# Kernel tuning notes

Hardware: AMD Instinct MI355X
Metric: run time of the kernel (lower is better)

Reference implementation:

```python
import jax, jax.numpy as jnp
import numpy as np

H, KVH, D, HID = 32, 8, 128, 4096
ROPE_LEN, THETA = 8192, 10000.0
MASK_OUT, MIN_REMAIN = 0.9, 128


def _rope_tables(dtype):
    inv_freq = 1.0 / (THETA ** (jnp.arange(0, D, 2, dtype=jnp.float32) / D))
    freqs = jnp.arange(ROPE_LEN, dtype=jnp.float32)[:, None] * inv_freq[None, :]
    emb = jnp.concatenate([freqs, freqs], axis=-1)  # [8192, 128]
    return jnp.cos(emb).astype(dtype), jnp.sin(emb).astype(dtype)


def _rotate_half(x):
    x1, x2 = x[..., : D // 2], x[..., D // 2:]
    return jnp.concatenate([-x2, x1], axis=-1)


def _apply_rope(x, pos, cos, sin):
    c, s = cos[pos][None, None], sin[pos][None, None]  # [1,1,L,D]
    return x * c + _rotate_half(x) * s


def setup_inputs() -> dict:
    key = jax.random.key(0)
    ks = jax.random.split(key, 11)
    S = 4096
    f = jnp.float32
    return {
        "hidden_states": jax.random.normal(ks[0], (1, 1, HID), f),
        "key_cache": jax.random.normal(ks[1], (1, H, S, D), f),
        "val_cache": jax.random.normal(ks[2], (1, H, S, D), f),
        "Wq": jax.random.normal(ks[3], (HID, HID), f) * 0.02,
        "Wk": jax.random.normal(ks[4], (HID, KVH * D), f) * 0.02,
        "Wv": jax.random.normal(ks[5], (HID, KVH * D), f) * 0.02,
        "Wo": jax.random.normal(ks[6], (HID, HID), f) * 0.02,
        "hash_proj1": jax.random.normal(ks[7], (1, H, D, D), f) * 0.001,
        "hash_bias1": jnp.zeros((1, H, 1, D), f),
        "hash_proj2": jax.random.normal(ks[8], (1, H, D, D), f) * 0.001,
        "hash_bias2": jnp.zeros((1, H, 1, D), f),
    }


def reference(hidden_states, key_cache, val_cache, Wq, Wk, Wv, Wo,
              hash_proj1, hash_bias1, hash_proj2, hash_bias2):
    B, Q, _ = hidden_states.shape  # B=1, Q=1 (decode step)
    G = H // KVH
    dtype = hidden_states.dtype

    # projections -> [B, heads, Q, D]
    ques = (hidden_states @ Wq).reshape(B, Q, H, D).transpose(0, 2, 1, 3)
    k_new = (hidden_states @ Wk).reshape(B, Q, KVH, D).transpose(0, 2, 1, 3)
    v_new = (hidden_states @ Wv).reshape(B, Q, KVH, D).transpose(0, 2, 1, 3)
    k_new = jnp.repeat(k_new, G, axis=1)  # repeat_kv
    v_new = jnp.repeat(v_new, G, axis=1)

    keys = jnp.concatenate([key_cache, k_new], axis=2)  # [1,H,K,D]
    vals = jnp.concatenate([val_cache, v_new], axis=2)
    K = keys.shape[2]

    cos, sin = _rope_tables(dtype)
    q_pos = K - Q + jnp.arange(Q)
    k_pos = jnp.arange(K)
    q_r = _apply_rope(ques, q_pos, cos, sin)
    k_r = _apply_rope(keys, k_pos, cos, sin)

    # per-head hash MLP: silu layer with residue, then linear layer with residue
    def hash_fn(x):
        h = jax.nn.silu(jnp.einsum('bhld,bhde->bhle', x, hash_proj1) + hash_bias1) + x
        h = (jnp.einsum('bhld,bhde->bhle', h, hash_proj2) + hash_bias2) + h
        return h

    q_hash = jnp.sign(hash_fn(q_r))
    k_hash = jnp.sign(hash_fn(k_r))
    draft_score = jnp.einsum('bhqd,bhkd->bhqk', q_hash, k_hash)  # LSH similarity

    num_remain = max(min(K, MIN_REMAIN), K - int(K * MASK_OUT))
    _, idx = jax.lax.top_k(draft_score, num_remain)  # [B,H,Q,num_remain]

    neg = jnp.finfo(dtype).min
    mask = jnp.full((B, H, Q, K), neg, dtype=dtype)
    bi = jnp.arange(B)[:, None, None, None]
    hi = jnp.arange(H)[None, :, None, None]
    qi = jnp.arange(Q)[None, None, :, None]
    mask = mask.at[bi, hi, qi, idx].set(0.0)

    scores = jnp.einsum('bhqd,bhkd->bhqk', q_r, k_r) / np.sqrt(D) + mask
    attn = jax.nn.softmax(scores, axis=-1)
    out = jnp.einsum('bhqk,bhkd->bhqd', attn, vals)
    out = out.transpose(0, 2, 1, 3).reshape(B, Q, HID) @ Wo
    return out
```

## Files before the change

### kernel.cpp

```cpp
#include <hip/hip_runtime.h>
#include <math.h>

#define NH 32
#define NKVH 8
#define HD 128

typedef _Float16 half8 __attribute__((ext_vector_type(8)));
typedef float f32x4 __attribute__((ext_vector_type(4)));

#define OFF_QPROJ 0
#define OFF_KNEW  4096
#define OFF_VNEW  5120
#define OFF_QR    6144
#define OFF_QHASH 10240
#define OFF_TAB   10368

__global__ void init_kernel(const float* __restrict__ hp1, const float* __restrict__ hp2,
                            float* __restrict__ ws, float* __restrict__ out,
                            int K, int nInit) {
    const int tid = threadIdx.x;
    if ((int)blockIdx.x < nInit) {
        int idx = blockIdx.x * 256 + tid;
        if (idx < K * 64) {
            int pos = idx >> 6, d = idx & 63;
            double inv = exp(-((double)d / 64.0) * log(10000.0));
            double ang = (double)pos * inv;
            double s, c;
            sincos(ang, &s, &c);
            ws[OFF_TAB + idx]                  = (float)c;
            ws[OFF_TAB + (size_t)K * 64 + idx] = (float)s;
        }
        if (idx < 6144) ws[OFF_QPROJ + idx] = 0.f;
        if (idx < 4096) out[idx] = 0.f;
        size_t off_attn = OFF_TAB + 2 * (size_t)K * 64 + 2 * (size_t)NH * K;
        if (idx < 4096) ws[off_attn + idx] = 0.f;
    } else {
        int id = blockIdx.x - nInit;
        int h2 = id >> 3;
        int tg = (id & 7) * 256 + tid;
        const int lane = tg & 63, nt = (tg >> 6) & 7, ks = tg >> 9;
        const int kbase = ks * 32 + ((tg >> 4) & 3) * 8;
        const int n = nt * 16 + (tg & 15);
        const float* P = ((h2 & 1) ? hp2 : hp1) + (size_t)(h2 >> 1) * 16384;
        half8 v;
#pragma unroll
        for (int j = 0; j < 8; ++j) v[j] = (_Float16)P[(size_t)(kbase + j) * 128 + n];
        size_t off_pt = OFF_TAB + 2 * (size_t)K * 64 + 2 * (size_t)NH * K + 4096 + 2 * (size_t)NH * 512;
        ((half8*)(ws + off_pt))[(size_t)h2 * 2048 + tg] = v;
    }
}

__global__ __launch_bounds__(256) void qkv_gemv(const float* __restrict__ hidden,
        const float* __restrict__ Wq, const float* __restrict__ Wk,
        const float* __restrict__ Wv, float* __restrict__ ws) {
    __shared__ float hs[64];
    const int tid = threadIdx.x;
    const int col = (blockIdx.x * 256 + tid) * 4;
    const int i0  = blockIdx.y * 64;
    if (tid < 64) hs[tid] = hidden[i0 + tid];
    __syncthreads();
    const float* W; int ld, wcol;
    if (col < 4096)      { W = Wq; ld = 4096; wcol = col; }
    else if (col < 5120) { W = Wk; ld = 1024; wcol = col - 4096; }
    else                 { W = Wv; ld = 1024; wcol = col - 5120; }
    const float* p = W + (size_t)i0 * ld + wcol;
    float4 a0 = {0.f,0.f,0.f,0.f}, a1 = {0.f,0.f,0.f,0.f};
#pragma unroll 4
    for (int ii = 0; ii < 64; ii += 2) {
        float4 w0 = *(const float4*)p;
        float4 w1 = *(const float4*)(p + ld);
        float h0 = hs[ii], h1 = hs[ii + 1];
        a0.x = fmaf(h0, w0.x, a0.x); a0.y = fmaf(h0, w0.y, a0.y);
        a0.z = fmaf(h0, w0.z, a0.z); a0.w = fmaf(h0, w0.w, a0.w);
        a1.x = fmaf(h1, w1.x, a1.x); a1.y = fmaf(h1, w1.y, a1.y);
        a1.z = fmaf(h1, w1.z, a1.z); a1.w = fmaf(h1, w1.w, a1.w);
        p += 2 * (size_t)ld;
    }
    atomicAdd(&ws[OFF_QPROJ + col + 0], a0.x + a1.x);
    atomicAdd(&ws[OFF_QPROJ + col + 1], a0.y + a1.y);
    atomicAdd(&ws[OFF_QPROJ + col + 2], a0.z + a1.z);
    atomicAdd(&ws[OFF_QPROJ + col + 3], a0.w + a1.w);
}

__global__ __launch_bounds__(128) void qhash_kernel(const float* __restrict__ hp1,
        const float* __restrict__ hb1, const float* __restrict__ hp2,
        const float* __restrict__ hb2, float* __restrict__ ws, int S) {
    const int h = blockIdx.x, d = threadIdx.x;
    const int K = S + 1;
    __shared__ float X[128], H1[128];
    float q  = ws[OFF_QPROJ + h * 128 + d];
    float qp = ws[OFF_QPROJ + h * 128 + (d ^ 64)];
    const float* cosT = ws + OFF_TAB;
    const float* sinT = cosT + (size_t)K * 64;
    float cs = cosT[(size_t)S * 64 + (d & 63)];
    float sn = sinT[(size_t)S * 64 + (d & 63)];
    float r = (d < 64) ? -qp : qp;
    float qr = q * cs + r * sn;
    X[d] = qr;
    ws[OFF_QR + h * 128 + d] = qr;
    __syncthreads();
    const float* P1 = hp1 + (size_t)h * 16384;
    float t = hb1[h * 128 + d];
    for (int i = 0; i < 128; ++i) t = fmaf(X[i], P1[i * 128 + d], t);
    float u = t / (1.f + expf(-t)) + X[d];
    H1[d] = u;
    __syncthreads();
    const float* P2 = hp2 + (size_t)h * 16384;
    float t2 = hb2[h * 128 + d] + u;
    for (int i = 0; i < 128; ++i) t2 = fmaf(H1[i], P2[i * 128 + d], t2);
    unsigned long long bal = __ballot(t2 > 0.f);
    if ((d & 63) == 0)
        ((unsigned long long*)(ws + OFF_QHASH))[h * 2 + (d >> 6)] = bal;
}

__global__ __launch_bounds__(256, 3) void key_kernel(const float* __restrict__ key_cache,
        const float* __restrict__ hb1, const float* __restrict__ hb2,
        float* __restrict__ ws, int S) {
    const int K  = S + 1;
    const int h  = blockIdx.y;
    const int k0 = blockIdx.x * 64;
    const int tid = threadIdx.x;
    const int wv = tid >> 6, lane = tid & 63;
    const int m = lane & 15, quad = lane >> 4;

    __shared__ float    XF[64 * 132];
    __shared__ _Float16 XH[64 * 136];

    const float* cosT = ws + OFF_TAB;
    const float* sinT = cosT + (size_t)K * 64;
    float* scores = ws + OFF_TAB + 2 * (size_t)K * 64;
    int*   draft  = (int*)(scores + (size_t)NH * K);
    size_t off_pt = OFF_TAB + 2 * (size_t)K * 64 + 2 * (size_t)NH * K + 4096 + 2 * (size_t)NH * 512;
    const half8* PT1 = (const half8*)((const _Float16*)(ws + off_pt) + (size_t)(h * 2) * 16384);
    const half8* PT2 = PT1 + 2048;

    const int key = tid >> 2, qq = tid & 3, d0 = qq * 16;
    const int kg = k0 + key;
    float lo[16], hi[16];
    if (kg < K) {
        const float* row = (kg < S) ? key_cache + ((size_t)h * S + kg) * 128
                                    : ws + OFF_KNEW + (h >> 2) * 128;
#pragma unroll
        for (int i4 = 0; i4 < 4; ++i4) {
            float4 xa = *(const float4*)(row + d0 + i4 * 4);
            float4 xb = *(const float4*)(row + 64 + d0 + i4 * 4);
            float4 cc = *(const float4*)(cosT + (size_t)kg * 64 + d0 + i4 * 4);
            float4 ss = *(const float4*)(sinT + (size_t)kg * 64 + d0 + i4 * 4);
            lo[i4*4+0] = xa.x * cc.x - xb.x * ss.x;  hi[i4*4+0] = xb.x * cc.x + xa.x * ss.x;
            lo[i4*4+1] = xa.y * cc.y - xb.y * ss.y;  hi[i4*4+1] = xb.y * cc.y + xa.y * ss.y;
            lo[i4*4+2] = xa.z * cc.z - xb.z * ss.z;  hi[i4*4+2] = xb.z * cc.z + xa.z * ss.z;
            lo[i4*4+3] = xa.w * cc.w - xb.w * ss.w;  hi[i4*4+3] = xb.w * cc.w + xa.w * ss.w;
        }
    } else {
#pragma unroll
        for (int i = 0; i < 16; ++i) { lo[i] = 0.f; hi[i] = 0.f; }
    }
#pragma unroll
    for (int i4 = 0; i4 < 4; ++i4) {
        float4 l4 = {lo[i4*4], lo[i4*4+1], lo[i4*4+2], lo[i4*4+3]};
        float4 h4 = {hi[i4*4], hi[i4*4+1], hi[i4*4+2], hi[i4*4+3]};
        *(float4*)&XF[key * 132 + d0 + i4 * 4]      = l4;
        *(float4*)&XF[key * 132 + 64 + d0 + i4 * 4] = h4;
    }
    {
        half8 hl0, hl1, hh0, hh1;
#pragma unroll
        for (int i = 0; i < 8; ++i) {
            hl0[i] = (_Float16)lo[i];     hl1[i] = (_Float16)lo[8 + i];
            hh0[i] = (_Float16)hi[i];     hh1[i] = (_Float16)hi[8 + i];
        }
        *(half8*)&XH[key * 136 + d0]          = hl0;
        *(half8*)&XH[key * 136 + d0 + 8]      = hl1;
        *(half8*)&XH[key * 136 + 64 + d0]     = hh0;
        *(half8*)&XH[key * 136 + 64 + d0 + 8] = hh1;
    }

    {
        const float* qr = ws + OFF_QR + h * 128;
        float part = 0.f;
#pragma unroll
        for (int i4 = 0; i4 < 4; ++i4) {
            float4 qa = *(const float4*)(qr + d0 + i4 * 4);
            float4 qb = *(const float4*)(qr + 64 + d0 + i4 * 4);
            part = fmaf(qa.x, lo[i4*4+0], fmaf(qb.x, hi[i4*4+0], part));
            part = fmaf(qa.y, lo[i4*4+1], fmaf(qb.y, hi[i4*4+1], part));
            part = fmaf(qa.z, lo[i4*4+2], fmaf(qb.z, hi[i4*4+2], part));
            part = fmaf(qa.w, lo[i4*4+3], fmaf(qb.w, hi[i4*4+3], part));
        }
        part += __shfl_xor(part, 1);
        part += __shfl_xor(part, 2);
        if (qq == 0 && kg < K) scores[(size_t)h * K + kg] = part * 0.08838834764831845f;
    }

    float b1v[8], b2v[8];
#pragma unroll
    for (int nt = 0; nt < 8; ++nt) {
        b1v[nt] = hb1[h * 128 + nt * 16 + m];
        b2v[nt] = hb2[h * 128 + nt * 16 + m];
    }
    unsigned short qh16[8];
    {
        uint4 q4 = *(const uint4*)((const unsigned*)(ws + OFF_QHASH) + h * 4);
        unsigned qa[4] = {q4.x, q4.y, q4.z, q4.w};
#pragma unroll
        for (int nt = 0; nt < 8; ++nt)
            qh16[nt] = (unsigned short)((qa[nt >> 1] >> ((nt & 1) * 16)) & 0xFFFFu);
    }

    f32x4 acc[8];

#define GEMM_MFMA(PT)                                                              \
    {                                                                              \
        _Pragma("unroll") for (int nt = 0; nt < 8; ++nt)                           \
            acc[nt] = (f32x4){0.f, 0.f, 0.f, 0.f};                                 \
        _Pragma("unroll") for (int c = 0; c < 4; ++c) {                            \
            half8 afrag = *(const half8*)&XH[(wv * 16 + m) * 136 + c * 32 + quad * 8]; \
            _Pragma("unroll") for (int nt = 0; nt < 8; ++nt) {                     \
                half8 bfrag = (PT)[c * 512 + nt * 64 + lane];                      \
                acc[nt] = __builtin_amdgcn_mfma_f32_16x16x32_f16(afrag, bfrag, acc[nt], 0, 0, 0); \
            }                                                                      \
        }                                                                          \
    }

    GEMM_MFMA(PT1)
#pragma unroll
    for (int nt = 0; nt < 8; ++nt) {
        const int n = nt * 16 + m;
#pragma unroll
        for (int r = 0; r < 4; ++r) {
            const int kk = wv * 16 + quad * 4 + r;
            float t = acc[nt][r] + b1v[nt];
            float x = XF[kk * 132 + n];
            float h1v = t / (1.f + expf(-t)) + x;
            XF[kk * 132 + n] = h1v;
            XH[kk * 136 + n] = (_Float16)h1v;
        }
    }

    GEMM_MFMA(PT2)
    {
        int ham[4] = {0, 0, 0, 0};
#pragma unroll
        for (int nt = 0; nt < 8; ++nt) {
            const int n = nt * 16 + m;
#pragma unroll
            for (int r = 0; r < 4; ++r) {
                const int kk = wv * 16 + quad * 4 + r;
                float t2 = acc[nt][r] + b2v[nt] + XF[kk * 132 + n];
                unsigned long long bal = __ballot(t2 > 0.f);
                unsigned bits = (unsigned)(bal >> (quad * 16)) & 0xFFFFu;
                ham[r] += __popc(bits ^ (unsigned)qh16[nt]);
            }
        }
        if (m == 0) {
#pragma unroll
            for (int r = 0; r < 4; ++r) {
                int kgd = k0 + wv * 16 + quad * 4 + r;
                if (kgd < K) draft[(size_t)h * K + kgd] = 128 - 2 * ham[r];
            }
        }
    }
#undef GEMM_MFMA
}

__global__ __launch_bounds__(256) void select_kernel(float* __restrict__ ws, int S, int nrem) {
    const int K = S + 1;
    const int h = blockIdx.x;
    const int tid = threadIdx.x;
    __shared__ int hist[129];
    __shared__ int sel_idx[512];
    __shared__ float red[256];
    __shared__ int wtot[4];
    __shared__ int sh_tval, sh_r, sh_cnt, sh_run;

    float* scoresB = ws + OFF_TAB + 2 * (size_t)K * 64;
    const int* draft = (const int*)(scoresB + (size_t)NH * K) + (size_t)h * K;
    const float* sc = scoresB + (size_t)h * K;
    float* attn = scoresB + 2 * (size_t)NH * K;
    int*   selidx_g = (int*)(attn + 4096) + h * 512;
    float* selw_g   = (attn + 4096 + NH * 512) + h * 512;

    for (int i = tid; i < 129; i += 256) hist[i] = 0;
    if (tid == 0) { sh_cnt = 0; sh_run = 0; }
    __syncthreads();
    for (int k = tid; k < K; k += 256) atomicAdd(&hist[(draft[k] + 128) >> 1], 1);
    __syncthreads();
    if (tid == 0) {
        int cum = 0, tb = 0, r = nrem;
        for (int b = 128; b >= 0; --b) {
            int c = hist[b];
            if (cum + c >= nrem) { tb = b; r = nrem - cum; break; }
            cum += c;
        }
        sh_tval = tb * 2 - 128; sh_r = r;
    }
    __syncthreads();
    const int tval = sh_tval, r = sh_r;
    const int lane = tid & 63, wave = tid >> 6;
    for (int base = 0; base < K; base += 256) {
        int k = base + tid;
        bool valid = (k < K);
        int dv = valid ? draft[k] : -1000;
        bool eq = valid && (dv == tval);
        bool gt = valid && (dv > tval);
        unsigned long long bal = __ballot(eq);
        if (lane == 0) wtot[wave] = __popcll(bal);
        __syncthreads();
        int woff = 0;
        for (int w = 0; w < wave; ++w) woff += wtot[w];
        int rank = sh_run + woff + __popcll(bal & ((1ull << lane) - 1ull));
        bool sel = gt || (eq && (rank < r));
        if (sel) sel_idx[atomicAdd(&sh_cnt, 1)] = k;
        __syncthreads();
        if (tid == 0) sh_run += wtot[0] + wtot[1] + wtot[2] + wtot[3];
        __syncthreads();
    }
    float mmax = -3.402823466e38f;
    for (int li = tid; li < nrem; li += 256) mmax = fmaxf(mmax, sc[sel_idx[li]]);
    red[tid] = mmax; __syncthreads();
    for (int s2 = 128; s2 > 0; s2 >>= 1) {
        if (tid < s2) red[tid] = fmaxf(red[tid], red[tid + s2]);
        __syncthreads();
    }
    mmax = red[0]; __syncthreads();
    float z = 0.f;
    for (int li = tid; li < nrem; li += 256) z += expf(sc[sel_idx[li]] - mmax);
    red[tid] = z; __syncthreads();
    for (int s2 = 128; s2 > 0; s2 >>= 1) {
        if (tid < s2) red[tid] += red[tid + s2];
        __syncthreads();
    }
    float Z = red[0]; __syncthreads();
    for (int li = tid; li < nrem; li += 256) {
        int idx = sel_idx[li];
        selidx_g[li] = idx;
        selw_g[li] = expf(sc[idx] - mmax) / Z;
    }
}

__global__ __launch_bounds__(256) void gather_kernel(const float* __restrict__ val_cache,
        float* __restrict__ ws, int S, int nrem) {
    const int K = S + 1;
    const int h = blockIdx.x, g = blockIdx.y;
    const int tid = threadIdx.x;
    const int wave = tid >> 6, lane = tid & 63;
    const int stream = g * 4 + wave;
    float* scoresB = ws + OFF_TAB + 2 * (size_t)K * 64;
    float* attn = scoresB + 2 * (size_t)NH * K;
    const int*   selidx_g = (const int*)(attn + 4096) + h * 512;
    const float* selw_g   = (attn + 4096 + NH * 512) + h * 512;
    float ax = 0.f, ay = 0.f;
    for (int li = stream; li < nrem; li += 64) {
        int idx = selidx_g[li];
        float w = selw_g[li];
        const float* vr = (idx < S) ? val_cache + ((size_t)h * S + idx) * 128
                                    : ws + OFF_VNEW + (h >> 2) * 128;
        float2 v = ((const float2*)vr)[lane];
        ax = fmaf(w, v.x, ax);
        ay = fmaf(w, v.y, ay);
    }
    atomicAdd(&attn[h * 128 + lane * 2 + 0], ax);
    atomicAdd(&attn[h * 128 + lane * 2 + 1], ay);
}

__global__ __launch_bounds__(256) void out_gemv(const float* __restrict__ Wo,
        const float* __restrict__ ws, float* __restrict__ out, int K) {
    __shared__ float hs[64];
    const int tid = threadIdx.x;
    const int col = (blockIdx.x * 256 + tid) * 4;
    const int i0  = blockIdx.y * 64;
    const float* ao = ws + OFF_TAB + 2 * (size_t)K * 64 + 2 * (size_t)NH * K;
    if (tid < 64) hs[tid] = ao[i0 + tid];
    __syncthreads();
    const float* p = Wo + (size_t)i0 * 4096 + col;
    float4 a0 = {0.f,0.f,0.f,0.f}, a1 = {0.f,0.f,0.f,0.f};
#pragma unroll 4
    for (int ii = 0; ii < 64; ii += 2) {
        float4 w0 = *(const float4*)p;
        float4 w1 = *(const float4*)(p + 4096);
        float h0 = hs[ii], h1 = hs[ii + 1];
        a0.x = fmaf(h0, w0.x, a0.x); a0.y = fmaf(h0, w0.y, a0.y);
        a0.z = fmaf(h0, w0.z, a0.z); a0.w = fmaf(h0, w0.w, a0.w);
        a1.x = fmaf(h1, w1.x, a1.x); a1.y = fmaf(h1, w1.y, a1.y);
        a1.z = fmaf(h1, w1.z, a1.z); a1.w = fmaf(h1, w1.w, a1.w);
        p += 8192;
    }
    atomicAdd(&out[col + 0], a0.x + a1.x);
    atomicAdd(&out[col + 1], a0.y + a1.y);
    atomicAdd(&out[col + 2], a0.z + a1.z);
    atomicAdd(&out[col + 3], a0.w + a1.w);
}

extern "C" void kernel_launch(void* const* d_in, const int* in_sizes, int n_in,
                              void* d_out, int out_size, void* d_ws, size_t ws_size,
                              hipStream_t stream) {
    const float* hidden = (const float*)d_in[0];
    const float* key_cache = (const float*)d_in[1];
    const float* val_cache = (const float*)d_in[2];
    const float* Wq = (const float*)d_in[3];
    const float* Wk = (const float*)d_in[4];
    const float* Wv = (const float*)d_in[5];
    const float* Wo = (const float*)d_in[6];
    const float* hp1 = (const float*)d_in[7];
    const float* hb1 = (const float*)d_in[8];
    const float* hp2 = (const float*)d_in[9];
    const float* hb2 = (const float*)d_in[10];
    float* out = (float*)d_out;
    float* ws  = (float*)d_ws;

    const int S = in_sizes[1] / (NH * HD);
    const int K = S + 1;
    int mn = (K < 128) ? K : 128;
    int nrem = K - (int)((double)K * 0.9);
    if (nrem < mn) nrem = mn;

    const int nInit = (K * 64 + 255) / 256;
    init_kernel<<<nInit + 512, 256, 0, stream>>>(hp1, hp2, ws, out, K, nInit);
    qkv_gemv<<<dim3(6, 64), 256, 0, stream>>>(hidden, Wq, Wk, Wv, ws);
    qhash_kernel<<<NH, 128, 0, stream>>>(hp1, hb1, hp2, hb2, ws, S);
    key_kernel<<<dim3((K + 63) / 64, NH), 256, 0, stream>>>(key_cache, hb1, hb2, ws, S);
    select_kernel<<<NH, 256, 0, stream>>>(ws, S, nrem);
    gather_kernel<<<dim3(NH, 16), 256, 0, stream>>>(val_cache, ws, S, nrem);
    out_gemv<<<dim3(4, 64), 256, 0, stream>>>(Wo, ws, out, K);
}
```

Baseline: 346.1 us.

## Process two key tiles per block with prefetch, direct MFMA fragments, swizzled LDS

key_kernel now handles 128 keys per block as two 64-key tiles, loading the second tile's key rows before the first tile is processed so global latency overlaps compute. Each lane loads its key data directly in MFMA A-fragment layout, which removes the fp16 shared staging buffer, and the fp32 LDS buffer uses an XOR swizzle instead of padding. Shared memory shrinks and occupancy bounds rise to 4, at the cost of more registers held for the prefetched tile and half as many blocks.

```diff
diff --git a/kernel.cpp b/kernel.cpp
--- a/kernel.cpp
+++ b/kernel.cpp
@@ -113,18 +113,20 @@
         ((unsigned long long*)(ws + OFF_QHASH))[h * 2 + (d >> 6)] = bal;
 }
 
-__global__ __launch_bounds__(256, 3) void key_kernel(const float* __restrict__ key_cache,
+__global__ __launch_bounds__(256, 4) void key_kernel(const float* __restrict__ key_cache,
         const float* __restrict__ hb1, const float* __restrict__ hb2,
         float* __restrict__ ws, int S) {
     const int K  = S + 1;
     const int h  = blockIdx.y;
-    const int k0 = blockIdx.x * 64;
+    const int k0 = blockIdx.x * 128;
     const int tid = threadIdx.x;
     const int wv = tid >> 6, lane = tid & 63;
     const int m = lane & 15, quad = lane >> 4;
-
-    __shared__ float    XF[64 * 132];
-    __shared__ _Float16 XH[64 * 136];
+    const int row = wv * 16 + m;
+    const int cbase = quad * 8;
+    const int sw = (m & 7) << 2;
+
+    __shared__ float XF[64 * 128];
 
     const float* cosT = ws + OFF_TAB;
     const float* sinT = cosT + (size_t)K * 64;
@@ -134,70 +136,119 @@
     const half8* PT1 = (const half8*)((const _Float16*)(ws + off_pt) + (size_t)(h * 2) * 16384);
     const half8* PT2 = PT1 + 2048;
 
-    const int key = tid >> 2, qq = tid & 3, d0 = qq * 16;
-    const int kg = k0 + key;
-    float lo[16], hi[16];
-    if (kg < K) {
-        const float* row = (kg < S) ? key_cache + ((size_t)h * S + kg) * 128
-                                    : ws + OFF_KNEW + (h >> 2) * 128;
-#pragma unroll
-        for (int i4 = 0; i4 < 4; ++i4) {
-            float4 xa = *(const float4*)(row + d0 + i4 * 4);
-            float4 xb = *(const float4*)(row + 64 + d0 + i4 * 4);
-            float4 cc = *(const float4*)(cosT + (size_t)kg * 64 + d0 + i4 * 4);
-            float4 ss = *(const float4*)(sinT + (size_t)kg * 64 + d0 + i4 * 4);
-            lo[i4*4+0] = xa.x * cc.x - xb.x * ss.x;  hi[i4*4+0] = xb.x * cc.x + xa.x * ss.x;
-            lo[i4*4+1] = xa.y * cc.y - xb.y * ss.y;  hi[i4*4+1] = xb.y * cc.y + xa.y * ss.y;
-            lo[i4*4+2] = xa.z * cc.z - xb.z * ss.z;  hi[i4*4+2] = xb.z * cc.z + xa.z * ss.z;
-            lo[i4*4+3] = xa.w * cc.w - xb.w * ss.w;  hi[i4*4+3] = xb.w * cc.w + xa.w * ss.w;
-        }
-    } else {
-#pragma unroll
-        for (int i = 0; i < 16; ++i) { lo[i] = 0.f; hi[i] = 0.f; }
-    }
-#pragma unroll
-    for (int i4 = 0; i4 < 4; ++i4) {
-        float4 l4 = {lo[i4*4], lo[i4*4+1], lo[i4*4+2], lo[i4*4+3]};
-        float4 h4 = {hi[i4*4], hi[i4*4+1], hi[i4*4+2], hi[i4*4+3]};
-        *(float4*)&XF[key * 132 + d0 + i4 * 4]      = l4;
-        *(float4*)&XF[key * 132 + 64 + d0 + i4 * 4] = h4;
-    }
-    {
-        half8 hl0, hl1, hh0, hh1;
-#pragma unroll
-        for (int i = 0; i < 8; ++i) {
-            hl0[i] = (_Float16)lo[i];     hl1[i] = (_Float16)lo[8 + i];
-            hh0[i] = (_Float16)hi[i];     hh1[i] = (_Float16)hi[8 + i];
-        }
-        *(half8*)&XH[key * 136 + d0]          = hl0;
-        *(half8*)&XH[key * 136 + d0 + 8]      = hl1;
-        *(half8*)&XH[key * 136 + 64 + d0]     = hh0;
-        *(half8*)&XH[key * 136 + 64 + d0 + 8] = hh1;
-    }
-
-    {
-        const float* qr = ws + OFF_QR + h * 128;
-        float part = 0.f;
-#pragma unroll
-        for (int i4 = 0; i4 < 4; ++i4) {
-            float4 qa = *(const float4*)(qr + d0 + i4 * 4);
-            float4 qb = *(const float4*)(qr + 64 + d0 + i4 * 4);
-            part = fmaf(qa.x, lo[i4*4+0], fmaf(qb.x, hi[i4*4+0], part));
-            part = fmaf(qa.y, lo[i4*4+1], fmaf(qb.y, hi[i4*4+1], part));
-            part = fmaf(qa.z, lo[i4*4+2], fmaf(qb.z, hi[i4*4+2], part));
-            part = fmaf(qa.w, lo[i4*4+3], fmaf(qb.w, hi[i4*4+3], part));
-        }
-        part += __shfl_xor(part, 1);
-        part += __shfl_xor(part, 2);
-        if (qq == 0 && kg < K) scores[(size_t)h * K + kg] = part * 0.08838834764831845f;
-    }
-
-    float b1v[8], b2v[8];
-#pragma unroll
-    for (int nt = 0; nt < 8; ++nt) {
-        b1v[nt] = hb1[h * 128 + nt * 16 + m];
-        b2v[nt] = hb2[h * 128 + nt * 16 + m];
-    }
+#define LOAD_KEYS(kgv, xv)                                                         \
+    if ((kgv) < K) {                                                               \
+        const float* krow_ = ((kgv) < S) ? key_cache + ((size_t)h * S + (kgv)) * 128 \
+                                         : ws + OFF_KNEW + (h >> 2) * 128;         \
+        _Pragma("unroll") for (int c = 0; c < 4; ++c) {                            \
+            *(float4*)&(xv)[c][0] = *(const float4*)(krow_ + c * 32 + cbase);      \
+            *(float4*)&(xv)[c][4] = *(const float4*)(krow_ + c * 32 + cbase + 4);  \
+        }                                                                          \
+    } else {                                                                       \
+        _Pragma("unroll") for (int c = 0; c < 4; ++c)                              \
+            _Pragma("unroll") for (int j = 0; j < 8; ++j) (xv)[c][j] = 0.f;        \
+    }
+
+#define ROPE_INPLACE(kgv, xv)                                                      \
+    if ((kgv) < K) {                                                               \
+        float cc_[2][8], ss_[2][8];                                                \
+        _Pragma("unroll") for (int c = 0; c < 2; ++c) {                            \
+            *(float4*)&cc_[c][0] = *(const float4*)(cosT + (size_t)(kgv) * 64 + c * 32 + cbase);     \
+            *(float4*)&cc_[c][4] = *(const float4*)(cosT + (size_t)(kgv) * 64 + c * 32 + cbase + 4); \
+            *(float4*)&ss_[c][0] = *(const float4*)(sinT + (size_t)(kgv) * 64 + c * 32 + cbase);     \
+            *(float4*)&ss_[c][4] = *(const float4*)(sinT + (size_t)(kgv) * 64 + c * 32 + cbase + 4); \
+        }                                                                          \
+        _Pragma("unroll") for (int c = 0; c < 2; ++c)                              \
+            _Pragma("unroll") for (int j = 0; j < 8; ++j) {                        \
+                float lo_ = (xv)[c][j] * cc_[c][j] - (xv)[c + 2][j] * ss_[c][j];   \
+                float hi_ = (xv)[c + 2][j] * cc_[c][j] + (xv)[c][j] * ss_[c][j];   \
+                (xv)[c][j] = lo_; (xv)[c + 2][j] = hi_;                            \
+            }                                                                      \
+    }
+
+#define PROCESS_TILE(xr, ktile)                                                    \
+    {                                                                              \
+        _Pragma("unroll") for (int c = 0; c < 4; ++c) {                            \
+            *(float4*)&XF[row * 128 + ((c * 32 + cbase) ^ sw)]     = *(float4*)&(xr)[c][0]; \
+            *(float4*)&XF[row * 128 + ((c * 32 + cbase + 4) ^ sw)] = *(float4*)&(xr)[c][4]; \
+        }                                                                          \
+        {                                                                          \
+            const float* qr_ = ws + OFF_QR + h * 128;                              \
+            float part = 0.f;                                                      \
+            _Pragma("unroll") for (int c = 0; c < 4; ++c) {                        \
+                float4 qa = *(const float4*)(qr_ + c * 32 + cbase);                \
+                float4 qb = *(const float4*)(qr_ + c * 32 + cbase + 4);            \
+                part = fmaf(qa.x, (xr)[c][0], part); part = fmaf(qa.y, (xr)[c][1], part); \
+                part = fmaf(qa.z, (xr)[c][2], part); part = fmaf(qa.w, (xr)[c][3], part); \
+                part = fmaf(qb.x, (xr)[c][4], part); part = fmaf(qb.y, (xr)[c][5], part); \
+                part = fmaf(qb.z, (xr)[c][6], part); part = fmaf(qb.w, (xr)[c][7], part); \
+            }                                                                      \
+            part += __shfl_xor(part, 16);                                          \
+            part += __shfl_xor(part, 32);                                          \
+            int kg_ = (ktile) + row;                                               \
+            if (quad == 0 && kg_ < K) scores[(size_t)h * K + kg_] = part * 0.08838834764831845f; \
+        }                                                                          \
+        half8 af_[4];                                                              \
+        _Pragma("unroll") for (int c = 0; c < 4; ++c)                              \
+            _Pragma("unroll") for (int j = 0; j < 8; ++j) af_[c][j] = (_Float16)(xr)[c][j]; \
+        f32x4 acc[8];                                                              \
+        _Pragma("unroll") for (int nt = 0; nt < 8; ++nt) acc[nt] = (f32x4){0.f,0.f,0.f,0.f}; \
+        _Pragma("unroll") for (int c = 0; c < 4; ++c)                              \
+            _Pragma("unroll") for (int nt = 0; nt < 8; ++nt)                       \
+                acc[nt] = __builtin_amdgcn_mfma_f32_16x16x32_f16(af_[c], PT1[c * 512 + nt * 64 + lane], acc[nt], 0, 0, 0); \
+        _Pragma("unroll") for (int nt = 0; nt < 8; ++nt) {                         \
+            const int n = nt * 16 + m;                                             \
+            float b1v = hb1[h * 128 + n];                                          \
+            _Pragma("unroll") for (int r = 0; r < 4; ++r) {                        \
+                const int kk = wv * 16 + quad * 4 + r;                             \
+                const int nn = n ^ ((kk & 7) << 2);                                \
+                float t = acc[nt][r] + b1v;                                        \
+                float x = XF[kk * 128 + nn];                                       \
+                XF[kk * 128 + nn] = t / (1.f + expf(-t)) + x;                      \
+            }                                                                      \
+        }                                                                          \
+        _Pragma("unroll") for (int nt = 0; nt < 8; ++nt) acc[nt] = (f32x4){0.f,0.f,0.f,0.f}; \
+        _Pragma("unroll") for (int c = 0; c < 4; ++c) {                            \
+            float4 f0 = *(const float4*)&XF[row * 128 + ((c * 32 + cbase) ^ sw)];  \
+            float4 f1 = *(const float4*)&XF[row * 128 + ((c * 32 + cbase + 4) ^ sw)]; \
+            half8 a2;                                                              \
+            a2[0] = (_Float16)f0.x; a2[1] = (_Float16)f0.y;                        \
+            a2[2] = (_Float16)f0.z; a2[3] = (_Float16)f0.w;                        \
+            a2[4] = (_Float16)f1.x; a2[5] = (_Float16)f1.y;                        \
+            a2[6] = (_Float16)f1.z; a2[7] = (_Float16)f1.w;                        \
+            _Pragma("unroll") for (int nt = 0; nt < 8; ++nt)                       \
+                acc[nt] = __builtin_amdgcn_mfma_f32_16x16x32_f16(a2, PT2[c * 512 + nt * 64 + lane], acc[nt], 0, 0, 0); \
+        }                                                                          \
+        {                                                                          \
+            int ham[4] = {0, 0, 0, 0};                                             \
+            _Pragma("unroll") for (int nt = 0; nt < 8; ++nt) {                     \
+                const int n = nt * 16 + m;                                         \
+                float b2v = hb2[h * 128 + n];                                      \
+                _Pragma("unroll") for (int r = 0; r < 4; ++r) {                    \
+                    const int kk = wv * 16 + quad * 4 + r;                         \
+                    float t2 = acc[nt][r] + b2v + XF[kk * 128 + (n ^ ((kk & 7) << 2))]; \
+                    unsigned long long bal = __ballot(t2 > 0.f);                   \
+                    unsigned bits = (unsigned)(bal >> (quad * 16)) & 0xFFFFu;      \
+                    ham[r] += __popc(bits ^ (unsigned)qh16[nt]);                   \
+                }                                                                  \
+            }                                                                      \
+            if (m == 0) {                                                          \
+                _Pragma("unroll") for (int r = 0; r < 4; ++r) {                    \
+                    int kgd = (ktile) + wv * 16 + quad * 4 + r;                    \
+                    if (kgd < K) draft[(size_t)h * K + kgd] = 128 - 2 * ham[r];    \
+                }                                                                  \
+            }                                                                      \
+        }                                                                          \
+    }
+
+    const int kgA = k0 + row, kgB = k0 + 64 + row;
+
+    float xrA[4][8];
+    LOAD_KEYS(kgA, xrA)
+    float xvB[4][8];
+    LOAD_KEYS(kgB, xvB)
+    ROPE_INPLACE(kgA, xrA)
+
     unsigned short qh16[8];
     {
         uint4 q4 = *(const uint4*)((const unsigned*)(ws + OFF_QHASH) + h * 4);
@@ -207,60 +258,14 @@
             qh16[nt] = (unsigned short)((qa[nt >> 1] >> ((nt & 1) * 16)) & 0xFFFFu);
     }
 
-    f32x4 acc[8];
-
-#define GEMM_MFMA(PT)                                                              \
-    {                                                                              \
-        _Pragma("unroll") for (int nt = 0; nt < 8; ++nt)                           \
-            acc[nt] = (f32x4){0.f, 0.f, 0.f, 0.f};                                 \
-        _Pragma("unroll") for (int c = 0; c < 4; ++c) {                            \
-            half8 afrag = *(const half8*)&XH[(wv * 16 + m) * 136 + c * 32 + quad * 8]; \
-            _Pragma("unroll") for (int nt = 0; nt < 8; ++nt) {                     \
-                half8 bfrag = (PT)[c * 512 + nt * 64 + lane];                      \
-                acc[nt] = __builtin_amdgcn_mfma_f32_16x16x32_f16(afrag, bfrag, acc[nt], 0, 0, 0); \
-            }                                                                      \
-        }                                                                          \
-    }
-
-    GEMM_MFMA(PT1)
-#pragma unroll
-    for (int nt = 0; nt < 8; ++nt) {
-        const int n = nt * 16 + m;
-#pragma unroll
-        for (int r = 0; r < 4; ++r) {
-            const int kk = wv * 16 + quad * 4 + r;
-            float t = acc[nt][r] + b1v[nt];
-            float x = XF[kk * 132 + n];
-            float h1v = t / (1.f + expf(-t)) + x;
-            XF[kk * 132 + n] = h1v;
-            XH[kk * 136 + n] = (_Float16)h1v;
-        }
-    }
-
-    GEMM_MFMA(PT2)
-    {
-        int ham[4] = {0, 0, 0, 0};
-#pragma unroll
-        for (int nt = 0; nt < 8; ++nt) {
-            const int n = nt * 16 + m;
-#pragma unroll
-            for (int r = 0; r < 4; ++r) {
-                const int kk = wv * 16 + quad * 4 + r;
-                float t2 = acc[nt][r] + b2v[nt] + XF[kk * 132 + n];
-                unsigned long long bal = __ballot(t2 > 0.f);
-                unsigned bits = (unsigned)(bal >> (quad * 16)) & 0xFFFFu;
-                ham[r] += __popc(bits ^ (unsigned)qh16[nt]);
-            }
-        }
-        if (m == 0) {
-#pragma unroll
-            for (int r = 0; r < 4; ++r) {
-                int kgd = k0 + wv * 16 + quad * 4 + r;
-                if (kgd < K) draft[(size_t)h * K + kgd] = 128 - 2 * ham[r];
-            }
-        }
-    }
-#undef GEMM_MFMA
+    PROCESS_TILE(xrA, k0)
+
+    ROPE_INPLACE(kgB, xvB)
+    PROCESS_TILE(xvB, k0 + 64)
+
+#undef LOAD_KEYS
+#undef ROPE_INPLACE
+#undef PROCESS_TILE
 }
 
 __global__ __launch_bounds__(256) void select_kernel(float* __restrict__ ws, int S, int nrem) {
@@ -418,7 +423,7 @@
     init_kernel<<<nInit + 512, 256, 0, stream>>>(hp1, hp2, ws, out, K, nInit);
     qkv_gemv<<<dim3(6, 64), 256, 0, stream>>>(hidden, Wq, Wk, Wv, ws);
     qhash_kernel<<<NH, 128, 0, stream>>>(hp1, hb1, hp2, hb2, ws, S);
-    key_kernel<<<dim3((K + 63) / 64, NH), 256, 0, stream>>>(key_cache, hb1, hb2, ws, S);
+    key_kernel<<<dim3((K + 127) / 128, NH), 256, 0, stream>>>(key_cache, hb1, hb2, ws, S);
     select_kernel<<<NH, 256, 0, stream>>>(ws, S, nrem);
     gather_kernel<<<dim3(NH, 16), 256, 0, stream>>>(val_cache, ws, S, nrem);
     out_gemv<<<dim3(4, 64), 256, 0, stream>>>(Wo, ws, out, K);
```

Result: slower. 441.4 us (+27.5%).
